# Optimization experiments

Measured on AMD Instinct MI355X. Metric: run time of the kernel, lower is better.

Reference implementation:

```python
import jax, jax.numpy as jnp
import numpy as np

D_MODEL, D_STATE, D_CONV, D_INNER, DT_RANK = 1024, 16, 4, 2048, 64
B_SZ, L = 2, 2048


def setup_inputs() -> dict:
    key = jax.random.key(0)
    ks = jax.random.split(key, 12)
    s = 0.02
    return {
        "x": jax.random.normal(ks[0], (B_SZ, L, D_MODEL), jnp.float32),
        "in_proj_w": jax.random.normal(ks[1], (2 * D_INNER, D_MODEL), jnp.float32) * s,
        "conv_w": jax.random.normal(ks[2], (D_INNER, 1, D_CONV), jnp.float32) * 0.1,
        "conv_b": jnp.zeros((D_INNER,), jnp.float32),
        "A_log": jax.random.normal(ks[3], (D_INNER, D_STATE), jnp.float32) * 0.1,
        "D": jnp.ones((D_INNER,), jnp.float32),
        "dt_proj_w": jax.random.uniform(ks[4], (D_INNER, DT_RANK), jnp.float32, -DT_RANK ** -0.5, DT_RANK ** -0.5),
        "dt_proj_b": jax.random.uniform(ks[5], (D_INNER,), jnp.float32, -5.0, -3.0),
        "x_proj_w": jax.random.normal(ks[6], (DT_RANK, D_INNER), jnp.float32) * s,
        "B_proj_w": jax.random.normal(ks[7], (D_STATE, D_INNER), jnp.float32) * s,
        "C_proj_w": jax.random.normal(ks[8], (D_STATE, D_INNER), jnp.float32) * s,
        "out_proj_w": jax.random.normal(ks[9], (D_MODEL, D_INNER), jnp.float32) * s,
    }


def _causal_depthwise_conv(x, w, b):
    # x: (b, L, d_inner); w: (d_inner, 1, d_conv); left-pad (d_conv-1) zeros = conv1d(padding=d_conv-1)[..., :L]
    xt = jnp.transpose(x, (0, 2, 1))  # (b, d_inner, L)
    xt = jnp.pad(xt, ((0, 0), (0, 0), (w.shape[-1] - 1, 0)))
    out = jax.lax.conv_general_dilated(
        xt, w, window_strides=(1,), padding="VALID",
        dimension_numbers=("NCW", "OIW", "NCW"), feature_group_count=w.shape[0])
    return jnp.transpose(out + b[None, :, None], (0, 2, 1))  # (b, L, d_inner)


def _selective_scan(x, dt, A, B, C):
    # x, dt: (b, L, d_inner); A: (d_inner, d_state); B, C: (b, L, d_state)
    b, seq_len, d_inner = x.shape
    h0 = jnp.zeros((b, d_inner, A.shape[1]), x.dtype)

    def step(h, inp):
        xt, dtt, Bt, Ct = inp  # (b,di) (b,di) (b,ds) (b,ds)
        dte = dtt[..., None]                         # (b, di, 1)
        h = h + dte * (A[None] * h) + dte * (Bt[:, None, :] * xt[..., None])
        yt = jnp.einsum("bns,bs->bn", h, Ct)
        return h, yt

    inputs = (jnp.swapaxes(x, 0, 1), jnp.swapaxes(dt, 0, 1),
              jnp.swapaxes(B, 0, 1), jnp.swapaxes(C, 0, 1))
    _, y = jax.lax.scan(step, h0, inputs)
    return jnp.swapaxes(y, 0, 1)  # (b, L, d_inner)


def _forward(x, in_proj_w, conv_w, conv_b, A_log, D, dt_proj_w, dt_proj_b,
             x_proj_w, B_proj_w, C_proj_w, out_proj_w):
    xz = x @ in_proj_w.T                         # (b, L, 2*d_inner)
    x_in, z = jnp.split(xz, 2, axis=-1)
    x_conv = jax.nn.silu(_causal_depthwise_conv(x_in, conv_w, conv_b))
    dt = jax.nn.softplus((x_conv @ x_proj_w.T) @ dt_proj_w.T + dt_proj_b)
    B = x_conv @ B_proj_w.T                      # (b, L, d_state)
    C = x_conv @ C_proj_w.T
    A = -jnp.exp(A_log)
    y = _selective_scan(x_conv, dt, A, B, C)
    y = y + D[None, None, :] * x_conv
    y = y * jax.nn.silu(z)
    return y @ out_proj_w.T                      # (b, L, d_model)


def reference(x, in_proj_w, conv_w, conv_b, A_log, D, dt_proj_w, dt_proj_b,
              x_proj_w, B_proj_w, C_proj_w, out_proj_w):
    return _forward(x, in_proj_w, conv_w, conv_b, A_log, D, dt_proj_w, dt_proj_b,
                    x_proj_w, B_proj_w, C_proj_w, out_proj_w)
```

## Files before the change

### kernel.cpp

```cpp
#include <hip/hip_runtime.h>
#include <hip/hip_bf16.h>
#include <math.h>

using bf16 = __hip_bfloat16;
typedef short bf16x8 __attribute__((ext_vector_type(8)));
typedef float f32x4  __attribute__((ext_vector_type(4)));

#define DMODEL 1024
#define DSTATE 16
#define DCONV  4
#define DINNER 2048
#define DTRANK 64
#define BSZ    2
#define LSEQ   2048
#define MROWS  (BSZ*LSEQ)

#define NCHUNK 32
#define CHUNK  (LSEQ / NCHUNK)
#define DS_TOT (DINNER * DSTATE)
#define NBCX   96

__device__ __forceinline__ float cvt(float v) { return v; }
__device__ __forceinline__ float cvt(bf16 v)  { return __bfloat162float(v); }

template<typename T> __device__ __forceinline__ T sto(float v);
template<> __device__ __forceinline__ float sto<float>(float v) { return v; }
template<> __device__ __forceinline__ bf16  sto<bf16>(float v)  { return __float2bfloat16(v); }

__device__ __forceinline__ void gll16(const bf16* g, short* l)
{
    __builtin_amdgcn_global_load_lds(
        (const __attribute__((address_space(1))) unsigned int*)(const void*)g,
        (__attribute__((address_space(3))) unsigned int*)(void*)l,
        16, 0, 0);
}

__global__ __launch_bounds__(256)
void cvt_all(const float* __restrict__ a, const float* __restrict__ b,
             const float* __restrict__ c, const float* __restrict__ d,
             const float* __restrict__ xp, const float* __restrict__ Bp,
             const float* __restrict__ Cp,
             bf16* __restrict__ oa, bf16* __restrict__ ob, bf16* __restrict__ oc,
             bf16* __restrict__ od, bf16* __restrict__ obcx,
             int na, int nb, int nc, int nd, int nbcx)
{
    const int idx = (blockIdx.x * 256 + threadIdx.x) * 4;
    const float* src; bf16* dst; int off;
    if (idx < na)                      { src = a; dst = oa; off = idx; }
    else if (idx < na + nb)            { src = b; dst = ob; off = idx - na; }
    else if (idx < na + nb + nc)       { src = c; dst = oc; off = idx - na - nb; }
    else if (idx < na + nb + nc + nd)  { src = d; dst = od; off = idx - na - nb - nc; }
    else if (idx < na+nb+nc+nd+nbcx) {
        off = idx - na - nb - nc - nd;
        const int r = off >> 11, k = off & 2047;
        src = (r < 64) ? (xp + (size_t)r * 2048 + k)
            : (r < 80) ? (Bp + (size_t)(r - 64) * 2048 + k)
                       : (Cp + (size_t)(r - 80) * 2048 + k);
        src -= off;
        dst = obcx;
    } else return;
    const float4 v = *(const float4*)(src + off);
    dst[off + 0] = sto<bf16>(v.x); dst[off + 1] = sto<bf16>(v.y);
    dst[off + 2] = sto<bf16>(v.z); dst[off + 3] = sto<bf16>(v.w);
}

template<typename TO, int SPLITK, int EPI>
__global__ __launch_bounds__(256)
void gemm_mfma(const bf16* __restrict__ A, const bf16* __restrict__ W,
               TO* __restrict__ out, TO* __restrict__ out2,
               const float* __restrict__ bias,
               int M, int N, int K, int split, int kchunk)
{
    __shared__ __align__(16) short smem[16384];
    short* As = smem;
    short* Bs = smem + 8192;

    const int tid  = threadIdx.x;
    const int lane = tid & 63;
    const int wv   = tid >> 6;
    const int wm = (wv & 1) * 64;
    const int wn = (wv >> 1) * 64;
    const int m0 = blockIdx.y * 128;
    const int n0 = blockIdx.x * 128;

    const int p0 = wv * 64 + lane;
    const int p1 = p0 + 256;
    const int r0 = p0 >> 2, c0 = (p0 & 3) ^ ((r0 >> 1) & 3);
    const int r1 = p1 >> 2, c1 = (p1 & 3) ^ ((r1 >> 1) & 3);

    const bf16* srcA0 = A + (size_t)(m0 + r0) * K + c0 * 8;
    const bf16* srcA1 = A + (size_t)(m0 + r1) * K + c1 * 8;
    int nr0 = n0 + r0; if (nr0 >= N) nr0 = N - 1;
    int nr1 = n0 + r1; if (nr1 >= N) nr1 = N - 1;
    const bf16* srcB0 = W + (size_t)nr0 * K + c0 * 8;
    const bf16* srcB1 = W + (size_t)nr1 * K + c1 * 8;

    const int C4 = lane >> 4;
    const int fr = lane & 15;
    int aOff[4], bOff[4];
    #pragma unroll
    for (int i = 0; i < 4; ++i) {
        const int R = wm + i * 16 + fr;
        aOff[i] = R * 32 + ((C4 ^ ((R >> 1) & 3)) << 3);
    }
    #pragma unroll
    for (int j = 0; j < 4; ++j) {
        const int R = wn + j * 16 + fr;
        bOff[j] = R * 32 + ((C4 ^ ((R >> 1) & 3)) << 3);
    }

    f32x4 acc[4][4] = {};

    const int kb  = blockIdx.z * kchunk;
    const int nit = kchunk / 32;

    gll16(srcA0 + kb, &As[wv * 512]);
    gll16(srcA1 + kb, &As[(wv + 4) * 512]);
    gll16(srcB0 + kb, &Bs[wv * 512]);
    gll16(srcB1 + kb, &Bs[(wv + 4) * 512]);

    for (int it = 0; it < nit; ++it) {
        __syncthreads();
        const int p = it & 1;
        if (it + 1 < nit) {
            const int q  = p ^ 1;
            const int k1 = kb + (it + 1) * 32;
            gll16(srcA0 + k1, &As[q * 4096 + wv * 512]);
            gll16(srcA1 + k1, &As[q * 4096 + (wv + 4) * 512]);
            gll16(srcB0 + k1, &Bs[q * 4096 + wv * 512]);
            gll16(srcB1 + k1, &Bs[q * 4096 + (wv + 4) * 512]);
        }
        bf16x8 af[4], bfr[4];
        #pragma unroll
        for (int i = 0; i < 4; ++i) af[i]  = *(const bf16x8*)&As[p * 4096 + aOff[i]];
        #pragma unroll
        for (int j = 0; j < 4; ++j) bfr[j] = *(const bf16x8*)&Bs[p * 4096 + bOff[j]];
        #pragma unroll
        for (int i = 0; i < 4; ++i)
            #pragma unroll
            for (int j = 0; j < 4; ++j)
                acc[i][j] = __builtin_amdgcn_mfma_f32_16x16x32_bf16(af[i], bfr[j], acc[i][j], 0, 0, 0);
    }

    __syncthreads();

    const int rb = (lane >> 4) * 4;

    if constexpr (sizeof(TO) == 2) {
        bf16* cs = (bf16*)smem;
        #pragma unroll
        for (int i = 0; i < 4; ++i)
            #pragma unroll
            for (int j = 0; j < 4; ++j)
                #pragma unroll
                for (int r = 0; r < 4; ++r) {
                    const int m = wm + i * 16 + rb + r;
                    const int n = wn + j * 16 + fr;
                    float v = acc[i][j][r];
                    if (EPI == 1) {
                        v += bias[n0 + n];
                        v = (v > 20.f) ? v : log1pf(expf(v));
                    }
                    const int key = (m >> 2) & 3;
                    cs[m * 128 + (n ^ ((key & 1) << 4) ^ ((key >> 1) << 5))] = sto<bf16>(v);
                }
        __syncthreads();
        TO* ob; int nc0; int ostr;
        if (split > 0) {
            if (n0 < split) { ob = out;  nc0 = n0;         }
            else            { ob = out2; nc0 = n0 - split; }
            ostr = split;
        } else { ob = out; nc0 = n0; ostr = N; }
        #pragma unroll
        for (int g8 = 0; g8 < 8; ++g8) {
            const int G = tid + 256 * g8;
            const int mrow = G >> 4;
            const int cg = G & 15;
            const int key = (mrow >> 2) & 3;
            const int nst = (cg * 8) ^ ((key & 1) << 4) ^ ((key >> 1) << 5);
            if (n0 + nst < N) {
                const uint4 val = *(const uint4*)&cs[mrow * 128 + cg * 8];
                *(uint4*)&ob[(size_t)(m0 + mrow) * ostr + nc0 + nst] = val;
            }
        }
    } else {
        float* fs = (float*)smem;
        float* obase = SPLITK ? ((float*)out + (size_t)blockIdx.z * M * N) : (float*)out;
        #pragma unroll
        for (int ph = 0; ph < 2; ++ph) {
            __syncthreads();
            if ((wn >> 6) == ph) {
                #pragma unroll
                for (int i = 0; i < 4; ++i)
                    #pragma unroll
                    for (int j = 0; j < 4; ++j)
                        #pragma unroll
                        for (int r = 0; r < 4; ++r) {
                            const int m = wm + i * 16 + rb + r;
                            const int qq = j * 16 + fr;
                            fs[m * 64 + (qq ^ (((m >> 2) & 1) << 4))] = acc[i][j][r];
                        }
            }
            __syncthreads();
            #pragma unroll
            for (int g8 = 0; g8 < 8; ++g8) {
                const int G = tid + 256 * g8;
                const int mrow = G >> 4;
                const int cg = G & 15;
                const int qst = (cg * 4) ^ (((mrow >> 2) & 1) << 4);
                const int n_g = 64 * ph + qst;
                if (n0 + n_g < N) {
                    const float4 val = *(const float4*)&fs[mrow * 64 + cg * 4];
                    *(float4*)&obase[(size_t)(m0 + mrow) * N + n0 + n_g] = val;
                }
            }
        }
    }
}

__global__ __launch_bounds__(256)
void reduce_bcx(const float* __restrict__ P8, bf16* __restrict__ xr,
                float* __restrict__ BC)
{
    const int u = blockIdx.x * 256 + threadIdx.x;
    const int m = u / NBCX;
    const int n = u - m * NBCX;
    float s = 0.f;
    #pragma unroll
    for (int k = 0; k < 8; ++k) s += P8[(size_t)k * MROWS * NBCX + u];
    if (n < 64) xr[(size_t)m * 64 + n] = sto<bf16>(s);
    else        BC[(size_t)m * 32 + (n - 64)] = s;
}

__global__ __launch_bounds__(256)
void conv_silu(const bf16* __restrict__ x_in, const float* __restrict__ cw,
               const float* __restrict__ cb, bf16* __restrict__ x_conv)
{
    const size_t i8 = (size_t)(blockIdx.x * 256 + threadIdx.x) * 8;
    const int d = (int)(i8 & (DINNER - 1));
    const int t = (int)((i8 >> 11) & (LSEQ - 1));
    uint4 v[4];
    const uint4 z4 = make_uint4(0, 0, 0, 0);
    v[3] = *(const uint4*)(x_in + i8);
    v[2] = (t >= 1) ? *(const uint4*)(x_in + i8 - 1 * DINNER) : z4;
    v[1] = (t >= 2) ? *(const uint4*)(x_in + i8 - 2 * DINNER) : z4;
    v[0] = (t >= 3) ? *(const uint4*)(x_in + i8 - 3 * DINNER) : z4;
    const bf16* e0 = (const bf16*)&v[0];
    const bf16* e1 = (const bf16*)&v[1];
    const bf16* e2 = (const bf16*)&v[2];
    const bf16* e3 = (const bf16*)&v[3];
    bf16 ob[8];
    #pragma unroll
    for (int e = 0; e < 8; ++e) {
        const float4 w = *(const float4*)(cw + (size_t)(d + e) * 4);
        float a = cb[d + e];
        a = fmaf(w.x, cvt(e0[e]), a);
        a = fmaf(w.y, cvt(e1[e]), a);
        a = fmaf(w.z, cvt(e2[e]), a);
        a = fmaf(w.w, cvt(e3[e]), a);
        const float sig = 1.f / (1.f + __expf(-a));
        ob[e] = sto<bf16>(a * sig);
    }
    *(uint4*)(x_conv + i8) = *(const uint4*)ob;
}

__global__ __launch_bounds__(64)
void scan_phase_a(const bf16* __restrict__ x_conv, const bf16* __restrict__ dt,
                  const float* __restrict__ BC, const float* __restrict__ A_log,
                  float* __restrict__ hend, float* __restrict__ Pprod)
{
    const int lane = threadIdx.x;
    const int c = blockIdx.x;
    const int d = blockIdx.y * 64 + lane;
    const int b = blockIdx.z;

    float Af[DSTATE];
    #pragma unroll
    for (int s = 0; s < DSTATE; ++s) Af[s] = -__expf(A_log[d * DSTATE + s]);

    float h[DSTATE], P[DSTATE];
    #pragma unroll
    for (int s = 0; s < DSTATE; ++s) { h[s] = 0.f; P[s] = 1.f; }

    const size_t base = ((size_t)b * LSEQ + (size_t)c * CHUNK) * DINNER + d;
    const bf16* xp  = x_conv + base;
    const bf16* dtp = dt + base;
    const float* Bp = BC + ((size_t)b * LSEQ + (size_t)c * CHUNK) * 32;

    for (int t0 = 0; t0 < CHUNK; t0 += 4) {
        float xg[4], dtg[4];
        #pragma unroll
        for (int j = 0; j < 4; ++j) {
            xg[j]  = cvt(xp [(size_t)(t0 + j) * DINNER]);
            dtg[j] = cvt(dtp[(size_t)(t0 + j) * DINNER]);
        }
        #pragma unroll
        for (int j = 0; j < 4; ++j) {
            float Bv[DSTATE];
            const float* Br = Bp + (size_t)(t0 + j) * 32;
            *(float4*)(&Bv[0])  = *(const float4*)(Br + 0);
            *(float4*)(&Bv[4])  = *(const float4*)(Br + 4);
            *(float4*)(&Bv[8])  = *(const float4*)(Br + 8);
            *(float4*)(&Bv[12]) = *(const float4*)(Br + 12);
            const float dtv = dtg[j];
            const float dtx = dtv * xg[j];
            #pragma unroll
            for (int s = 0; s < DSTATE; ++s) {
                const float a = fmaf(dtv, Af[s], 1.0f);
                h[s] = fmaf(h[s], a, dtx * Bv[s]);
                P[s] *= a;
            }
        }
    }

    const size_t oidx = (((size_t)b * NCHUNK + c) * DINNER + d) * DSTATE;
    #pragma unroll
    for (int s = 0; s < DSTATE; ++s) {
        hend [oidx + s] = h[s];
        Pprod[oidx + s] = P[s];
    }
}

__global__ __launch_bounds__(256)
void scan_combine(float* __restrict__ hend, const float* __restrict__ Pprod)
{
    const int u = blockIdx.x * 256 + threadIdx.x;
    const int b = blockIdx.y;
    float h = 0.f;
    for (int c = 0; c < NCHUNK; ++c) {
        const size_t idx = ((size_t)b * NCHUNK + c) * DS_TOT + u;
        const float he = hend[idx];
        const float p  = Pprod[idx];
        hend[idx] = h;
        h = fmaf(p, h, he);
    }
}

__global__ __launch_bounds__(64)
void scan_phase_c(const bf16* __restrict__ x_conv, const bf16* __restrict__ dt,
                  const float* __restrict__ BC,
                  const float* __restrict__ A_log, const float* __restrict__ Dw,
                  const float* __restrict__ hin, bf16* __restrict__ zy)
{
    const int lane = threadIdx.x;
    const int c = blockIdx.x;
    const int d = blockIdx.y * 64 + lane;
    const int b = blockIdx.z;

    float Af[DSTATE];
    #pragma unroll
    for (int s = 0; s < DSTATE; ++s) Af[s] = -__expf(A_log[d * DSTATE + s]);
    const float Dv = Dw[d];

    float h[DSTATE];
    const size_t hidx = (((size_t)b * NCHUNK + c) * DINNER + d) * DSTATE;
    #pragma unroll
    for (int s = 0; s < DSTATE; ++s) h[s] = hin[hidx + s];

    const size_t base = ((size_t)b * LSEQ + (size_t)c * CHUNK) * DINNER + d;
    const bf16* xp  = x_conv + base;
    const bf16* dtp = dt + base;
    bf16*       zp  = zy + base;
    const float* Bp = BC + ((size_t)b * LSEQ + (size_t)c * CHUNK) * 32;
    const float* Cp = Bp + 16;

    for (int t0 = 0; t0 < CHUNK; t0 += 4) {
        float xg[4], dtg[4], zg[4];
        #pragma unroll
        for (int j = 0; j < 4; ++j) {
            xg[j]  = cvt(xp [(size_t)(t0 + j) * DINNER]);
            dtg[j] = cvt(dtp[(size_t)(t0 + j) * DINNER]);
            zg[j]  = cvt(zp [(size_t)(t0 + j) * DINNER]);
        }
        #pragma unroll
        for (int j = 0; j < 4; ++j) {
            float Bv[DSTATE], Cv[DSTATE];
            const float* Br = Bp + (size_t)(t0 + j) * 32;
            const float* Cr = Cp + (size_t)(t0 + j) * 32;
            *(float4*)(&Bv[0])  = *(const float4*)(Br + 0);
            *(float4*)(&Bv[4])  = *(const float4*)(Br + 4);
            *(float4*)(&Bv[8])  = *(const float4*)(Br + 8);
            *(float4*)(&Bv[12]) = *(const float4*)(Br + 12);
            *(float4*)(&Cv[0])  = *(const float4*)(Cr + 0);
            *(float4*)(&Cv[4])  = *(const float4*)(Cr + 4);
            *(float4*)(&Cv[8])  = *(const float4*)(Cr + 8);
            *(float4*)(&Cv[12]) = *(const float4*)(Cr + 12);
            const float dtv = dtg[j];
            const float dtx = dtv * xg[j];
            float y = 0.f;
            #pragma unroll
            for (int s = 0; s < DSTATE; ++s) {
                const float a = fmaf(dtv, Af[s], 1.0f);
                h[s] = fmaf(h[s], a, dtx * Bv[s]);
                y = fmaf(h[s], Cv[s], y);
            }
            const float zv = zg[j];
            const float sig = 1.f / (1.f + __expf(-zv));
            zp[(size_t)(t0 + j) * DINNER] = sto<bf16>(fmaf(Dv, xg[j], y) * (zv * sig));
        }
    }
}

extern "C" void kernel_launch(void* const* d_in, const int* in_sizes, int n_in,
                              void* d_out, int out_size, void* d_ws, size_t ws_size,
                              hipStream_t stream)
{
    const float* x          = (const float*)d_in[0];
    const float* in_proj_w  = (const float*)d_in[1];
    const float* conv_w     = (const float*)d_in[2];
    const float* conv_b     = (const float*)d_in[3];
    const float* A_log      = (const float*)d_in[4];
    const float* Dw         = (const float*)d_in[5];
    const float* dt_proj_w  = (const float*)d_in[6];
    const float* dt_proj_b  = (const float*)d_in[7];
    const float* x_proj_w   = (const float*)d_in[8];
    const float* B_proj_w   = (const float*)d_in[9];
    const float* C_proj_w   = (const float*)d_in[10];
    const float* out_proj_w = (const float*)d_in[11];
    float* out = (float*)d_out;

    const size_t MD = (size_t)MROWS * DINNER;
    bf16* buf0 = (bf16*)d_ws;
    bf16* buf1 = buf0 + MD;
    bf16* buf2 = buf1 + MD;
    bf16* xbf  = buf2 + MD;
    bf16* wbf1 = xbf  + (size_t)MROWS * DMODEL;
    bf16* wbf2 = wbf1 + (size_t)2 * DINNER * DMODEL;
    bf16* wbc  = wbf2 + (size_t)DMODEL * DINNER;
    bf16* wdt  = wbc  + (size_t)NBCX * DINNER;
    float* hend = (float*)(wdt + (size_t)DINNER * DTRANK);
    float* Pp   = hend + (size_t)BSZ * NCHUNK * DS_TOT;
    bf16*  xr_bf = xbf;
    float* BCbuf = (float*)(xbf + (size_t)MROWS * DTRANK);
    float* P8 = (float*)buf0;

    dim3 blk(256);
    const int na = MROWS * DMODEL;
    const int nb = 2 * DINNER * DMODEL;
    const int nc = DMODEL * DINNER;
    const int nd = DINNER * DTRANK;
    const int nbcx = NBCX * DINNER;

    cvt_all<<<(na + nb + nc + nd + nbcx) / 1024, blk, 0, stream>>>(
        x, in_proj_w, out_proj_w, dt_proj_w, x_proj_w, B_proj_w, C_proj_w,
        xbf, wbf1, wbf2, wdt, wbc, na, nb, nc, nd, nbcx);

    gemm_mfma<bf16, 0, 0><<<dim3(2 * DINNER / 128, MROWS / 128, 1), blk, 0, stream>>>(
        xbf, wbf1, buf0, buf1, nullptr, MROWS, 2 * DINNER, DMODEL, DINNER, DMODEL);

    conv_silu<<<(MROWS * DINNER) / (256 * 8), blk, 0, stream>>>(buf0, conv_w, conv_b, buf2);

    gemm_mfma<float, 1, 0><<<dim3(1, MROWS / 128, 8), blk, 0, stream>>>(
        buf2, wbc, P8, (float*)nullptr, nullptr, MROWS, NBCX, DINNER, 0, DINNER / 8);

    reduce_bcx<<<(MROWS * NBCX) / 256, blk, 0, stream>>>(P8, xr_bf, BCbuf);

    gemm_mfma<bf16, 0, 1><<<dim3(DINNER / 128, MROWS / 128, 1), blk, 0, stream>>>(
        xr_bf, wdt, buf0, (bf16*)nullptr, dt_proj_b, MROWS, DINNER, DTRANK, 0, DTRANK);

    scan_phase_a<<<dim3(NCHUNK, DINNER / 64, BSZ), dim3(64), 0, stream>>>(
        buf2, buf0, BCbuf, A_log, hend, Pp);
    scan_combine<<<dim3(DS_TOT / 256, BSZ), dim3(256), 0, stream>>>(hend, Pp);
    scan_phase_c<<<dim3(NCHUNK, DINNER / 64, BSZ), dim3(64), 0, stream>>>(
        buf2, buf0, BCbuf, A_log, Dw, hend, buf1);

    gemm_mfma<float, 0, 0><<<dim3(DMODEL / 128, MROWS / 128, 1), blk, 0, stream>>>(
        buf1, wbf2, out, (float*)nullptr, nullptr, MROWS, DMODEL, DINNER, 0, DINNER);
}
```

Before: 327.0 us.

## Split scan state across lane pairs and use narrower N tile for out_proj GEMM

```diff
diff --git a/kernel.cpp b/kernel.cpp
--- a/kernel.cpp
+++ b/kernel.cpp
@@ -64,13 +64,15 @@
     dst[off + 2] = sto<bf16>(v.z); dst[off + 3] = sto<bf16>(v.w);
 }
 
-template<typename TO, int SPLITK, int EPI>
+template<typename TO, int SPLITK, int EPI, int NBT>
 __global__ __launch_bounds__(256)
 void gemm_mfma(const bf16* __restrict__ A, const bf16* __restrict__ W,
                TO* __restrict__ out, TO* __restrict__ out2,
                const float* __restrict__ bias,
                int M, int N, int K, int split, int kchunk)
 {
+    constexpr int NJ = NBT / 32;
+    constexpr int BSTR = NBT * 32;
     __shared__ __align__(16) short smem[16384];
     short* As = smem;
     short* Bs = smem + 8192;
@@ -79,9 +81,9 @@
     const int lane = tid & 63;
     const int wv   = tid >> 6;
     const int wm = (wv & 1) * 64;
-    const int wn = (wv >> 1) * 64;
+    const int wn = (wv >> 1) * (NBT / 2);
     const int m0 = blockIdx.y * 128;
-    const int n0 = blockIdx.x * 128;
+    const int n0 = blockIdx.x * NBT;
 
     const int p0 = wv * 64 + lane;
     const int p1 = p0 + 256;
@@ -91,25 +93,28 @@
     const bf16* srcA0 = A + (size_t)(m0 + r0) * K + c0 * 8;
     const bf16* srcA1 = A + (size_t)(m0 + r1) * K + c1 * 8;
     int nr0 = n0 + r0; if (nr0 >= N) nr0 = N - 1;
-    int nr1 = n0 + r1; if (nr1 >= N) nr1 = N - 1;
     const bf16* srcB0 = W + (size_t)nr0 * K + c0 * 8;
-    const bf16* srcB1 = W + (size_t)nr1 * K + c1 * 8;
+    const bf16* srcB1 = nullptr;
+    if constexpr (NBT == 128) {
+        int nr1 = n0 + r1; if (nr1 >= N) nr1 = N - 1;
+        srcB1 = W + (size_t)nr1 * K + c1 * 8;
+    }
 
     const int C4 = lane >> 4;
     const int fr = lane & 15;
-    int aOff[4], bOff[4];
+    int aOff[4], bOff[NJ];
     #pragma unroll
     for (int i = 0; i < 4; ++i) {
         const int R = wm + i * 16 + fr;
         aOff[i] = R * 32 + ((C4 ^ ((R >> 1) & 3)) << 3);
     }
     #pragma unroll
-    for (int j = 0; j < 4; ++j) {
+    for (int j = 0; j < NJ; ++j) {
         const int R = wn + j * 16 + fr;
         bOff[j] = R * 32 + ((C4 ^ ((R >> 1) & 3)) << 3);
     }
 
-    f32x4 acc[4][4] = {};
+    f32x4 acc[4][NJ] = {};
 
     const int kb  = blockIdx.z * kchunk;
     const int nit = kchunk / 32;
@@ -117,7 +122,7 @@
     gll16(srcA0 + kb, &As[wv * 512]);
     gll16(srcA1 + kb, &As[(wv + 4) * 512]);
     gll16(srcB0 + kb, &Bs[wv * 512]);
-    gll16(srcB1 + kb, &Bs[(wv + 4) * 512]);
+    if constexpr (NBT == 128) gll16(srcB1 + kb, &Bs[(wv + 4) * 512]);
 
     for (int it = 0; it < nit; ++it) {
         __syncthreads();
@@ -127,18 +132,18 @@
             const int k1 = kb + (it + 1) * 32;
             gll16(srcA0 + k1, &As[q * 4096 + wv * 512]);
             gll16(srcA1 + k1, &As[q * 4096 + (wv + 4) * 512]);
-            gll16(srcB0 + k1, &Bs[q * 4096 + wv * 512]);
-            gll16(srcB1 + k1, &Bs[q * 4096 + (wv + 4) * 512]);
-        }
-        bf16x8 af[4], bfr[4];
+            gll16(srcB0 + k1, &Bs[q * BSTR + wv * 512]);
+            if constexpr (NBT == 128) gll16(srcB1 + k1, &Bs[q * BSTR + (wv + 4) * 512]);
+        }
+        bf16x8 af[4], bfr[NJ];
         #pragma unroll
         for (int i = 0; i < 4; ++i) af[i]  = *(const bf16x8*)&As[p * 4096 + aOff[i]];
         #pragma unroll
-        for (int j = 0; j < 4; ++j) bfr[j] = *(const bf16x8*)&Bs[p * 4096 + bOff[j]];
+        for (int j = 0; j < NJ; ++j) bfr[j] = *(const bf16x8*)&Bs[p * BSTR + bOff[j]];
         #pragma unroll
         for (int i = 0; i < 4; ++i)
             #pragma unroll
-            for (int j = 0; j < 4; ++j)
+            for (int j = 0; j < NJ; ++j)
                 acc[i][j] = __builtin_amdgcn_mfma_f32_16x16x32_bf16(af[i], bfr[j], acc[i][j], 0, 0, 0);
     }
 
@@ -151,7 +156,7 @@
         #pragma unroll
         for (int i = 0; i < 4; ++i)
             #pragma unroll
-            for (int j = 0; j < 4; ++j)
+            for (int j = 0; j < NJ; ++j)
                 #pragma unroll
                 for (int r = 0; r < 4; ++r) {
                     const int m = wm + i * 16 + rb + r;
@@ -162,7 +167,7 @@
                         v = (v > 20.f) ? v : log1pf(expf(v));
                     }
                     const int key = (m >> 2) & 3;
-                    cs[m * 128 + (n ^ ((key & 1) << 4) ^ ((key >> 1) << 5))] = sto<bf16>(v);
+                    cs[m * NBT + (n ^ ((key & 1) << 4) ^ ((key >> 1) << 5))] = sto<bf16>(v);
                 }
         __syncthreads();
         TO* ob; int nc0; int ostr;
@@ -171,46 +176,49 @@
             else            { ob = out2; nc0 = n0 - split; }
             ostr = split;
         } else { ob = out; nc0 = n0; ostr = N; }
-        #pragma unroll
-        for (int g8 = 0; g8 < 8; ++g8) {
+        constexpr int GPR = NBT / 8;
+        #pragma unroll
+        for (int g8 = 0; g8 < NBT / 16; ++g8) {
             const int G = tid + 256 * g8;
-            const int mrow = G >> 4;
-            const int cg = G & 15;
+            const int mrow = G / GPR;
+            const int cg = G % GPR;
             const int key = (mrow >> 2) & 3;
             const int nst = (cg * 8) ^ ((key & 1) << 4) ^ ((key >> 1) << 5);
             if (n0 + nst < N) {
-                const uint4 val = *(const uint4*)&cs[mrow * 128 + cg * 8];
+                const uint4 val = *(const uint4*)&cs[mrow * NBT + cg * 8];
                 *(uint4*)&ob[(size_t)(m0 + mrow) * ostr + nc0 + nst] = val;
             }
         }
     } else {
         float* fs = (float*)smem;
         float* obase = SPLITK ? ((float*)out + (size_t)blockIdx.z * M * N) : (float*)out;
+        constexpr int HW = NBT / 2;
         #pragma unroll
         for (int ph = 0; ph < 2; ++ph) {
             __syncthreads();
-            if ((wn >> 6) == ph) {
+            if (wn / HW == ph) {
                 #pragma unroll
                 for (int i = 0; i < 4; ++i)
                     #pragma unroll
-                    for (int j = 0; j < 4; ++j)
+                    for (int j = 0; j < NJ; ++j)
                         #pragma unroll
                         for (int r = 0; r < 4; ++r) {
                             const int m = wm + i * 16 + rb + r;
                             const int qq = j * 16 + fr;
-                            fs[m * 64 + (qq ^ (((m >> 2) & 1) << 4))] = acc[i][j][r];
+                            fs[m * HW + (qq ^ (((m >> 2) & 1) << 4))] = acc[i][j][r];
                         }
             }
             __syncthreads();
+            constexpr int FPR = HW / 4;
             #pragma unroll
-            for (int g8 = 0; g8 < 8; ++g8) {
+            for (int g8 = 0; g8 < NBT / 16; ++g8) {
                 const int G = tid + 256 * g8;
-                const int mrow = G >> 4;
-                const int cg = G & 15;
+                const int mrow = G / FPR;
+                const int cg = G % FPR;
                 const int qst = (cg * 4) ^ (((mrow >> 2) & 1) << 4);
-                const int n_g = 64 * ph + qst;
+                const int n_g = HW * ph + qst;
                 if (n0 + n_g < N) {
-                    const float4 val = *(const float4*)&fs[mrow * 64 + cg * 4];
+                    const float4 val = *(const float4*)&fs[mrow * HW + cg * 4];
                     *(float4*)&obase[(size_t)(m0 + mrow) * N + n0 + n_g] = val;
                 }
             }
@@ -270,22 +278,24 @@
                   float* __restrict__ hend, float* __restrict__ Pprod)
 {
     const int lane = threadIdx.x;
+    const int sp = lane & 1;
+    const int d  = blockIdx.y * 32 + (lane >> 1);
     const int c = blockIdx.x;
-    const int d = blockIdx.y * 64 + lane;
     const int b = blockIdx.z;
-
-    float Af[DSTATE];
-    #pragma unroll
-    for (int s = 0; s < DSTATE; ++s) Af[s] = -__expf(A_log[d * DSTATE + s]);
-
-    float h[DSTATE], P[DSTATE];
-    #pragma unroll
-    for (int s = 0; s < DSTATE; ++s) { h[s] = 0.f; P[s] = 1.f; }
+    const int sb = sp * 8;
+
+    float Af[8];
+    #pragma unroll
+    for (int s = 0; s < 8; ++s) Af[s] = -__expf(A_log[d * DSTATE + sb + s]);
+
+    float h[8], P[8];
+    #pragma unroll
+    for (int s = 0; s < 8; ++s) { h[s] = 0.f; P[s] = 1.f; }
 
     const size_t base = ((size_t)b * LSEQ + (size_t)c * CHUNK) * DINNER + d;
     const bf16* xp  = x_conv + base;
     const bf16* dtp = dt + base;
-    const float* Bp = BC + ((size_t)b * LSEQ + (size_t)c * CHUNK) * 32;
+    const float* Bp = BC + ((size_t)b * LSEQ + (size_t)c * CHUNK) * 32 + sb;
 
     for (int t0 = 0; t0 < CHUNK; t0 += 4) {
         float xg[4], dtg[4];
@@ -296,16 +306,14 @@
         }
         #pragma unroll
         for (int j = 0; j < 4; ++j) {
-            float Bv[DSTATE];
+            float Bv[8];
             const float* Br = Bp + (size_t)(t0 + j) * 32;
-            *(float4*)(&Bv[0])  = *(const float4*)(Br + 0);
-            *(float4*)(&Bv[4])  = *(const float4*)(Br + 4);
-            *(float4*)(&Bv[8])  = *(const float4*)(Br + 8);
-            *(float4*)(&Bv[12]) = *(const float4*)(Br + 12);
+            *(float4*)(&Bv[0]) = *(const float4*)(Br + 0);
+            *(float4*)(&Bv[4]) = *(const float4*)(Br + 4);
             const float dtv = dtg[j];
             const float dtx = dtv * xg[j];
             #pragma unroll
-            for (int s = 0; s < DSTATE; ++s) {
+            for (int s = 0; s < 8; ++s) {
                 const float a = fmaf(dtv, Af[s], 1.0f);
                 h[s] = fmaf(h[s], a, dtx * Bv[s]);
                 P[s] *= a;
@@ -313,12 +321,11 @@
         }
     }
 
-    const size_t oidx = (((size_t)b * NCHUNK + c) * DINNER + d) * DSTATE;
-    #pragma unroll
-    for (int s = 0; s < DSTATE; ++s) {
-        hend [oidx + s] = h[s];
-        Pprod[oidx + s] = P[s];
-    }
+    const size_t oidx = (((size_t)b * NCHUNK + c) * DINNER + d) * DSTATE + sb;
+    *(float4*)&hend [oidx + 0] = *(const float4*)&h[0];
+    *(float4*)&hend [oidx + 4] = *(const float4*)&h[4];
+    *(float4*)&Pprod[oidx + 0] = *(const float4*)&P[0];
+    *(float4*)&Pprod[oidx + 4] = *(const float4*)&P[4];
 }
 
 __global__ __launch_bounds__(256)
@@ -343,25 +350,27 @@
                   const float* __restrict__ hin, bf16* __restrict__ zy)
 {
     const int lane = threadIdx.x;
+    const int sp = lane & 1;
+    const int d  = blockIdx.y * 32 + (lane >> 1);
     const int c = blockIdx.x;
-    const int d = blockIdx.y * 64 + lane;
     const int b = blockIdx.z;
-
-    float Af[DSTATE];
-    #pragma unroll
-    for (int s = 0; s < DSTATE; ++s) Af[s] = -__expf(A_log[d * DSTATE + s]);
+    const int sb = sp * 8;
+
+    float Af[8];
+    #pragma unroll
+    for (int s = 0; s < 8; ++s) Af[s] = -__expf(A_log[d * DSTATE + sb + s]);
     const float Dv = Dw[d];
 
-    float h[DSTATE];
-    const size_t hidx = (((size_t)b * NCHUNK + c) * DINNER + d) * DSTATE;
-    #pragma unroll
-    for (int s = 0; s < DSTATE; ++s) h[s] = hin[hidx + s];
+    float h[8];
+    const size_t hidx = (((size_t)b * NCHUNK + c) * DINNER + d) * DSTATE + sb;
+    *(float4*)&h[0] = *(const float4*)&hin[hidx + 0];
+    *(float4*)&h[4] = *(const float4*)&hin[hidx + 4];
 
     const size_t base = ((size_t)b * LSEQ + (size_t)c * CHUNK) * DINNER + d;
     const bf16* xp  = x_conv + base;
     const bf16* dtp = dt + base;
     bf16*       zp  = zy + base;
-    const float* Bp = BC + ((size_t)b * LSEQ + (size_t)c * CHUNK) * 32;
+    const float* Bp = BC + ((size_t)b * LSEQ + (size_t)c * CHUNK) * 32 + sb;
     const float* Cp = Bp + 16;
 
     for (int t0 = 0; t0 < CHUNK; t0 += 4) {
@@ -374,29 +383,28 @@
         }
         #pragma unroll
         for (int j = 0; j < 4; ++j) {
-            float Bv[DSTATE], Cv[DSTATE];
+            float Bv[8], Cv[8];
             const float* Br = Bp + (size_t)(t0 + j) * 32;
             const float* Cr = Cp + (size_t)(t0 + j) * 32;
-            *(float4*)(&Bv[0])  = *(const float4*)(Br + 0);
-            *(float4*)(&Bv[4])  = *(const float4*)(Br + 4);
-            *(float4*)(&Bv[8])  = *(const float4*)(Br + 8);
-            *(float4*)(&Bv[12]) = *(const float4*)(Br + 12);
-            *(float4*)(&Cv[0])  = *(const float4*)(Cr + 0);
-            *(float4*)(&Cv[4])  = *(const float4*)(Cr + 4);
-            *(float4*)(&Cv[8])  = *(const float4*)(Cr + 8);
-            *(float4*)(&Cv[12]) = *(const float4*)(Cr + 12);
+            *(float4*)(&Bv[0]) = *(const float4*)(Br + 0);
+            *(float4*)(&Bv[4]) = *(const float4*)(Br + 4);
+            *(float4*)(&Cv[0]) = *(const float4*)(Cr + 0);
+            *(float4*)(&Cv[4]) = *(const float4*)(Cr + 4);
             const float dtv = dtg[j];
             const float dtx = dtv * xg[j];
             float y = 0.f;
             #pragma unroll
-            for (int s = 0; s < DSTATE; ++s) {
+            for (int s = 0; s < 8; ++s) {
                 const float a = fmaf(dtv, Af[s], 1.0f);
                 h[s] = fmaf(h[s], a, dtx * Bv[s]);
                 y = fmaf(h[s], Cv[s], y);
             }
-            const float zv = zg[j];
-            const float sig = 1.f / (1.f + __expf(-zv));
-            zp[(size_t)(t0 + j) * DINNER] = sto<bf16>(fmaf(Dv, xg[j], y) * (zv * sig));
+            y += __shfl_xor(y, 1);
+            if (sp == 0) {
+                const float zv = zg[j];
+                const float sig = 1.f / (1.f + __expf(-zv));
+                zp[(size_t)(t0 + j) * DINNER] = sto<bf16>(fmaf(Dv, xg[j], y) * (zv * sig));
+            }
         }
     }
 }
@@ -445,25 +453,25 @@
         x, in_proj_w, out_proj_w, dt_proj_w, x_proj_w, B_proj_w, C_proj_w,
         xbf, wbf1, wbf2, wdt, wbc, na, nb, nc, nd, nbcx);
 
-    gemm_mfma<bf16, 0, 0><<<dim3(2 * DINNER / 128, MROWS / 128, 1), blk, 0, stream>>>(
+    gemm_mfma<bf16, 0, 0, 128><<<dim3(2 * DINNER / 128, MROWS / 128, 1), blk, 0, stream>>>(
         xbf, wbf1, buf0, buf1, nullptr, MROWS, 2 * DINNER, DMODEL, DINNER, DMODEL);
 
     conv_silu<<<(MROWS * DINNER) / (256 * 8), blk, 0, stream>>>(buf0, conv_w, conv_b, buf2);
 
-    gemm_mfma<float, 1, 0><<<dim3(1, MROWS / 128, 8), blk, 0, stream>>>(
+    gemm_mfma<float, 1, 0, 128><<<dim3(1, MROWS / 128, 8), blk, 0, stream>>>(
         buf2, wbc, P8, (float*)nullptr, nullptr, MROWS, NBCX, DINNER, 0, DINNER / 8);
 
     reduce_bcx<<<(MROWS * NBCX) / 256, blk, 0, stream>>>(P8, xr_bf, BCbuf);
 
-    gemm_mfma<bf16, 0, 1><<<dim3(DINNER / 128, MROWS / 128, 1), blk, 0, stream>>>(
+    gemm_mfma<bf16, 0, 1, 128><<<dim3(DINNER / 128, MROWS / 128, 1), blk, 0, stream>>>(
         xr_bf, wdt, buf0, (bf16*)nullptr, dt_proj_b, MROWS, DINNER, DTRANK, 0, DTRANK);
 
-    scan_phase_a<<<dim3(NCHUNK, DINNER / 64, BSZ), dim3(64), 0, stream>>>(
+    scan_phase_a<<<dim3(NCHUNK, DINNER / 32, BSZ), dim3(64), 0, stream>>>(
         buf2, buf0, BCbuf, A_log, hend, Pp);
     scan_combine<<<dim3(DS_TOT / 256, BSZ), dim3(256), 0, stream>>>(hend, Pp);
-    scan_phase_c<<<dim3(NCHUNK, DINNER / 64, BSZ), dim3(64), 0, stream>>>(
+    scan_phase_c<<<dim3(NCHUNK, DINNER / 32, BSZ), dim3(64), 0, stream>>>(
         buf2, buf0, BCbuf, A_log, Dw, hend, buf1);
 
-    gemm_mfma<float, 0, 0><<<dim3(DMODEL / 128, MROWS / 128, 1), blk, 0, stream>>>(
+    gemm_mfma<float, 0, 0, 64><<<dim3(DMODEL / 64, MROWS / 128, 1), blk, 0, stream>>>(
         buf1, wbf2, out, (float*)nullptr, nullptr, MROWS, DMODEL, DINNER, 0, DINNER);
 }
```

Result: slower. 342.4 us (+4.7%).
